# Kernel optimization log

Measured on AMD Instinct MI355X. Metric: run time of the kernel, lower is better.

The kernel has to match this reference:

```python
import jax, jax.numpy as jnp
import numpy as np
import math

# dims (scaled-down DeepSeek-MLA-style config)
DIM = 2048
NH = 16
QLR = 768       # dla_q_lora_rank
KVLR = 512      # dla_kv_lora_rank
DN = 128        # qk_nope_head_dim
DR = 64         # qk_rope_head_dim
DV = 128        # v_head_dim
QKH = DN + DR   # 192
BSZ = 1
SEQ = 2048
LAYER_IDX = 3
LAMBDA_INIT = 0.8 - 0.6 * math.exp(-0.3 * LAYER_IDX)
SCALE = QKH ** -0.5  # max_seq_len == original_seq_len -> no mscale correction
MAX_SCORE = 100.0


def apply_rope(x, cos, sin):
    # x: [b, s, h, d]; consecutive pairs (x[2i], x[2i+1]) form complex numbers
    xr, xi = x[..., 0::2], x[..., 1::2]
    c = cos[None, :, None, :]
    sn = sin[None, :, None, :]
    yr = xr * c - xi * sn
    yi = xr * sn + xi * c
    return jnp.stack([yr, yi], axis=-1).reshape(x.shape)


def setup_inputs() -> dict:
    key = jax.random.key(0)
    ks = jax.random.split(key, 12)
    x = jax.random.normal(ks[0], (BSZ, SEQ, DIM), dtype=jnp.float32)
    s = 0.02
    wq_a = jax.random.normal(ks[1], (QLR, DIM), dtype=jnp.float32) * s
    wq_b = jax.random.normal(ks[2], (NH * QKH, QLR), dtype=jnp.float32) * s
    wkv_a = jax.random.normal(ks[3], (KVLR + DR, DIM), dtype=jnp.float32) * s
    wkv_b = jax.random.normal(ks[4], (NH * (DN + DV), KVLR), dtype=jnp.float32) * s
    wo = jax.random.normal(ks[5], (DIM, NH * DV), dtype=jnp.float32) * s
    lambda_q_nope = jax.random.normal(ks[6], (DN,), dtype=jnp.float32) * 0.1
    lambda_q_rope = jax.random.normal(ks[7], (DR,), dtype=jnp.float32) * 0.1
    lambda_k_nope = jax.random.normal(ks[8], (DN,), dtype=jnp.float32) * 0.1
    lambda_k_rope = jax.random.normal(ks[9], (DR,), dtype=jnp.float32) * 0.1
    # rope frequencies
    inv_freq = 1.0 / (10000.0 ** (np.arange(0, DR, 2, dtype=np.float32) / DR))
    angles = np.arange(SEQ, dtype=np.float32)[:, None] * inv_freq[None, :]
    freqs_cos = jnp.asarray(np.cos(angles))
    freqs_sin = jnp.asarray(np.sin(angles))
    # causal mask (prefill, start_pos = 0)
    mask = jnp.where(jnp.tril(jnp.ones((SEQ, SEQ), dtype=bool)), 0.0, -1e9).astype(jnp.float32)
    return {
        'x': x, 'wq_a': wq_a, 'wq_b': wq_b, 'wkv_a': wkv_a, 'wkv_b': wkv_b, 'wo': wo,
        'lambda_q_nope': lambda_q_nope, 'lambda_q_rope': lambda_q_rope,
        'lambda_k_nope': lambda_k_nope, 'lambda_k_rope': lambda_k_rope,
        'freqs_cos': freqs_cos, 'freqs_sin': freqs_sin, 'mask': mask, 'start_pos': 0,
    }


def reference(x, wq_a, wq_b, wkv_a, wkv_b, wo,
              lambda_q_nope, lambda_q_rope, lambda_k_nope, lambda_k_rope,
              freqs_cos, freqs_sin, mask, start_pos):
    b, s, _ = x.shape
    # differential-attention lambda scalar
    lam = (jnp.exp(jnp.dot(lambda_q_nope, lambda_k_nope))
           - jnp.exp(jnp.dot(lambda_q_rope, lambda_k_rope)) + LAMBDA_INIT)
    # low-rank q projection
    q = (x @ wq_a.T) @ wq_b.T                    # [b, s, NH*QKH]
    q = q.reshape(b, s, NH, QKH)
    q_nope, q_pe = q[..., :DN], q[..., DN:]
    q_pe = apply_rope(q_pe, freqs_cos, freqs_sin)
    # compressed kv + shared rope key
    kv_full = x @ wkv_a.T                        # [b, s, KVLR + DR]
    kv, k_pe = kv_full[..., :KVLR], kv_full[..., KVLR:]
    k_pe = apply_rope(k_pe[:, :, None, :], freqs_cos, freqs_sin)  # [b, s, 1, DR]
    kvb = (kv @ wkv_b.T).reshape(b, s, NH, DN + DV)
    k_nope, v = kvb[..., :DN], kvb[..., DN:]
    q_full = jnp.concatenate([q_nope, q_pe], axis=-1)             # [b, s, NH, 192]
    k_full = jnp.concatenate([k_nope, jnp.broadcast_to(k_pe, (b, s, NH, DR))], axis=-1)
    # differential split into two halves of qk_head_dim//2 = 96
    H = QKH // 2
    q1, q2 = q_full[..., :H], q_full[..., H:]
    k1, k2 = k_full[..., :H], k_full[..., H:]
    s1 = jnp.einsum('bshd,bthd->bhst', q1, k1) * SCALE
    s2 = jnp.einsum('bshd,bthd->bhst', q2, k2) * SCALE
    s1 = jnp.clip(s1, -MAX_SCORE, MAX_SCORE) + mask[None, None]
    s2 = jnp.clip(s2, -MAX_SCORE, MAX_SCORE) + mask[None, None]
    attn = jax.nn.softmax(s1, axis=-1) - lam * jax.nn.softmax(s2, axis=-1)
    out = jnp.einsum('bhst,bthd->bshd', attn, v)  # [b, s, NH, DV]
    out = out * (1.0 - LAMBDA_INIT)
    return out.reshape(b, s, NH * DV) @ wo.T
```

## Files before the change

### kernel.cpp

```cpp
#include <hip/hip_runtime.h>
#include <stdint.h>

#define SEQ   2048
#define NH    16
#define DIMM  2048
#define QLR   768
#define KVLR  512
#define DN    128
#define DR    64
#define DV    128
#define QKH   192
#define KVPAD 640
#define SCALE_F 0.07216878364870323f
#define LAM_INIT 0.5560582f
#define C1F      0.4439418f
#define PSTR  36
#define DTHR  8.0f

typedef __attribute__((ext_vector_type(8))) uint16_t u16x8;
typedef __attribute__((ext_vector_type(8))) __bf16   bf16x8;
typedef __attribute__((ext_vector_type(4))) float    f32x4;

#define MFMA16(a,b,c) __builtin_amdgcn_mfma_f32_16x16x32_bf16((a),(b),(c),0,0,0)

__device__ __forceinline__ uint16_t f2bf(float f){ uint32_t x; __builtin_memcpy(&x,&f,4); return (uint16_t)((x + 0x7FFFu + ((x>>16)&1u))>>16); }
__device__ __forceinline__ float bfu(uint16_t u){ return (float)__builtin_bit_cast(__bf16, u); }
__device__ __forceinline__ bf16x8 ldfrag(const uint16_t* p){ return __builtin_bit_cast(bf16x8, *(const u16x8*)p); }
__device__ __forceinline__ void gload_lds16(const uint16_t* g, uint16_t* l){
  __builtin_amdgcn_global_load_lds((const __attribute__((address_space(1))) void*)g,
                                   (__attribute__((address_space(3))) void*)l, 16, 0, 0);
}
__device__ __forceinline__ void stor(uint16_t* p, float v){ *p = f2bf(v); }
__device__ __forceinline__ void stor(float* p, float v){ *p = v; }

__global__ void cvt(const float* __restrict__ in, uint16_t* __restrict__ outp){
  int i = (blockIdx.x*256 + threadIdx.x)*8;
  float4 a = *(const float4*)(in + i);
  float4 b = *(const float4*)(in + i + 4);
  u16x8 r;
  r[0]=f2bf(a.x); r[1]=f2bf(a.y); r[2]=f2bf(a.z); r[3]=f2bf(a.w);
  r[4]=f2bf(b.x); r[5]=f2bf(b.y); r[6]=f2bf(b.z); r[7]=f2bf(b.w);
  *(u16x8*)(outp + i) = r;
}

__global__ void pad_wkva(const float* __restrict__ in, uint16_t* __restrict__ outp){
  int idx = blockIdx.x*256 + threadIdx.x;
  int n = idx >> 11;
  outp[idx] = (n < 576) ? f2bf(in[idx]) : (uint16_t)0;
}

template <typename OT>
__global__ __launch_bounds__(256) void gemm_bt(const uint16_t* __restrict__ A, int lda,
                                               const uint16_t* __restrict__ B,
                                               OT* __restrict__ C, int ldc, int K)
{
  __shared__ __align__(16) uint16_t As[128*32];
  __shared__ __align__(16) uint16_t Bs[128*32];
  const int tid  = threadIdx.x;
  const int wid  = tid >> 6;
  const int lane = tid & 63;
  const int wr   = (wid >> 1) * 64;
  const int wc   = (wid & 1) * 64;
  const int srow = lane >> 2;
  const int scol = (lane & 3) * 8;
  const uint16_t* Abase = A + (size_t)(blockIdx.x * 128) * lda;
  const uint16_t* Bbase = B + (size_t)(blockIdx.y * 128) * K;
  f32x4 acc[4][4] = {};
  for (int k0 = 0; k0 < K; k0 += 32) {
    __syncthreads();
#pragma unroll
    for (int c = 0; c < 2; ++c) {
      int r = (wid*2 + c)*16 + srow;
      gload_lds16(Abase + (size_t)r*lda + k0 + scol, &As[(wid*2 + c)*512]);
      gload_lds16(Bbase + (size_t)r*K   + k0 + scol, &Bs[(wid*2 + c)*512]);
    }
    __syncthreads();
    bf16x8 af[4], bfr[4];
#pragma unroll
    for (int m = 0; m < 4; ++m)
      af[m] = ldfrag(&As[(wr + m*16 + (lane&15))*32 + ((lane>>4)*8)]);
#pragma unroll
    for (int n = 0; n < 4; ++n)
      bfr[n] = ldfrag(&Bs[(wc + n*16 + (lane&15))*32 + ((lane>>4)*8)]);
#pragma unroll
    for (int m = 0; m < 4; ++m)
#pragma unroll
      for (int n = 0; n < 4; ++n)
        acc[m][n] = MFMA16(af[m], bfr[n], acc[m][n]);
  }
  const int rbase = blockIdx.x*128 + wr + ((lane>>4)<<2);
  const int cbase = blockIdx.y*128 + wc + (lane&15);
#pragma unroll
  for (int m = 0; m < 4; ++m)
#pragma unroll
    for (int n = 0; n < 4; ++n)
#pragma unroll
      for (int r = 0; r < 4; ++r)
        stor(&C[(size_t)(rbase + m*16 + r)*ldc + cbase + n*16], acc[m][n][r]);
}

__global__ __launch_bounds__(256) void gemm_kvb(const uint16_t* __restrict__ A, int lda,
                                                const uint16_t* __restrict__ B,
                                                uint16_t* __restrict__ kfull,
                                                uint16_t* __restrict__ vtb, int K)
{
  __shared__ __align__(16) uint16_t As[128*32];
  __shared__ __align__(16) uint16_t Bs[128*32];
  const int tid  = threadIdx.x;
  const int wid  = tid >> 6;
  const int lane = tid & 63;
  const int wr   = (wid >> 1) * 64;
  const int wc   = (wid & 1) * 64;
  const int srow = lane >> 2;
  const int scol = (lane & 3) * 8;
  const uint16_t* Abase = A + (size_t)(blockIdx.x * 128) * lda;
  const uint16_t* Bbase = B + (size_t)(blockIdx.y * 128) * K;
  f32x4 acc[4][4] = {};
  for (int k0 = 0; k0 < K; k0 += 32) {
    __syncthreads();
#pragma unroll
    for (int c = 0; c < 2; ++c) {
      int r = (wid*2 + c)*16 + srow;
      gload_lds16(Abase + (size_t)r*lda + k0 + scol, &As[(wid*2 + c)*512]);
      gload_lds16(Bbase + (size_t)r*K   + k0 + scol, &Bs[(wid*2 + c)*512]);
    }
    __syncthreads();
    bf16x8 af[4], bfr[4];
#pragma unroll
    for (int m = 0; m < 4; ++m)
      af[m] = ldfrag(&As[(wr + m*16 + (lane&15))*32 + ((lane>>4)*8)]);
#pragma unroll
    for (int n = 0; n < 4; ++n)
      bfr[n] = ldfrag(&Bs[(wc + n*16 + (lane&15))*32 + ((lane>>4)*8)]);
#pragma unroll
    for (int m = 0; m < 4; ++m)
#pragma unroll
      for (int n = 0; n < 4; ++n)
        acc[m][n] = MFMA16(af[m], bfr[n], acc[m][n]);
  }
  const int rbase = blockIdx.x*128 + wr + ((lane>>4)<<2);
  const int cbase = blockIdx.y*128 + wc + (lane&15);
#pragma unroll
  for (int m = 0; m < 4; ++m)
#pragma unroll
    for (int n = 0; n < 4; ++n) {
      const int gcol = cbase + n*16;
      const int hh = gcol >> 8, d = gcol & 255;
#pragma unroll
      for (int r = 0; r < 4; ++r) {
        const int t = rbase + m*16 + r;
        if (d < DN) kfull[((size_t)hh*SEQ + t)*QKH + d] = f2bf(acc[m][n][r]);
        else        vtb[((size_t)hh*DV + (d - DN))*SEQ + t] = f2bf(acc[m][n][r]);
      }
    }
}

__global__ void lam_kernel(const float* lqn, const float* lqr,
                           const float* lkn, const float* lkr, float* outp){
  if (threadIdx.x == 0 && blockIdx.x == 0) {
    float d1 = 0.f, d2 = 0.f;
    for (int i = 0; i < DN; ++i) d1 += lqn[i] * lkn[i];
    for (int i = 0; i < DR; ++i) d2 += lqr[i] * lkr[i];
    outp[0] = __expf(d1) - __expf(d2) + LAM_INIT;
  }
}

__global__ void rope_q(uint16_t* __restrict__ q, const float* __restrict__ cs,
                       const float* __restrict__ sn){
  int idx = blockIdx.x*256 + threadIdx.x;
  int j = idx & 31, hh = (idx>>5) & 15, s = idx >> 9;
  uint16_t* p = q + (size_t)s*(NH*QKH) + hh*QKH + DN + 2*j;
  float xr = bfu(p[0]), xi = bfu(p[1]);
  float c = cs[s*32+j], si = sn[s*32+j];
  p[0] = f2bf(xr*c - xi*si);
  p[1] = f2bf(xr*si + xi*c);
}

__global__ void rope_k(const uint16_t* __restrict__ kvf, const float* __restrict__ cs,
                       const float* __restrict__ sn, uint16_t* __restrict__ kfull){
  int idx = blockIdx.x*256 + threadIdx.x;
  int j = idx & 31, t = (idx>>5) & 2047, hh = idx >> 16;
  float xr = bfu(kvf[(size_t)t*KVPAD + KVLR + 2*j]);
  float xi = bfu(kvf[(size_t)t*KVPAD + KVLR + 2*j + 1]);
  float c = cs[t*32+j], si = sn[t*32+j];
  uint16_t* p = kfull + ((size_t)hh*SEQ + t)*QKH + DN + 2*j;
  p[0] = f2bf(xr*c - xi*si);
  p[1] = f2bf(xr*si + xi*c);
}

__global__ __launch_bounds__(256) __attribute__((amdgpu_waves_per_eu(2)))
void attn_kernel(
    const uint16_t* __restrict__ q,
    const uint16_t* __restrict__ kf,
    const uint16_t* __restrict__ vt,
    const float* __restrict__ lamp,
    uint16_t* __restrict__ o)
{
  __shared__ __align__(16) uint16_t P_lds[4][4][16*PSTR];
  __shared__ float R_lds[2][64*41];
  const int b  = blockIdx.x;
  const int h  = b & 15;
  const int c  = b >> 4;
  const int wid  = threadIdx.x >> 6;
  const int lane = threadIdx.x & 63;
  const int l15 = lane & 15;
  const int lhi = lane >> 4;
  const int subrow = lhi * 4;
  const int qrow0 = c * 16;
  const int kend  = qrow0 + 16;
  const float lam = lamp[0];

  bf16x8 qf[6];
  {
    const uint16_t* qbase = q + (size_t)(qrow0 + l15)*(NH*QKH) + h*QKH + lhi*8;
#pragma unroll
    for (int kb = 0; kb < 6; ++kb) qf[kb] = ldfrag(qbase + kb*32);
  }
  f32x4 O1[8] = {}, O2[8] = {};
  float m1[4], m2[4], l1[4], l2[4];
#pragma unroll
  for (int r = 0; r < 4; ++r) { m1[r] = m2[r] = -1e30f; l1[r] = l2[r] = 0.f; }

  const uint16_t* kbase = kf + (size_t)h*SEQ*QKH;
  const uint16_t* vbase = vt + (size_t)h*DV*SEQ;

  auto loadK = [&](bf16x8 (&k0)[6], bf16x8 (&k1)[6], int t0){
    const uint16_t* kp0 = kbase + (size_t)(t0 + l15)*QKH + lhi*8;
    const uint16_t* kp1 = kp0 + (size_t)16*QKH;
#pragma unroll
    for (int kb = 0; kb < 6; ++kb) { k0[kb] = ldfrag(kp0 + kb*32); k1[kb] = ldfrag(kp1 + kb*32); }
  };
  auto loadV = [&](bf16x8 (&vf)[8], int t0){
#pragma unroll
    for (int n = 0; n < 8; ++n) vf[n] = ldfrag(vbase + (size_t)(n*16 + l15)*SEQ + t0 + lhi*8);
  };
  auto qk = [&](bf16x8 (&k0)[6], bf16x8 (&k1)[6], f32x4 (&s1)[2], f32x4 (&s2)[2]){
    __builtin_amdgcn_s_setprio(1);
#pragma unroll
    for (int kb = 0; kb < 3; ++kb) { s1[0] = MFMA16(qf[kb], k0[kb], s1[0]); s1[1] = MFMA16(qf[kb], k1[kb], s1[1]); }
#pragma unroll
    for (int kb = 3; kb < 6; ++kb) { s2[0] = MFMA16(qf[kb], k0[kb], s2[0]); s2[1] = MFMA16(qf[kb], k1[kb], s2[1]); }
    __builtin_amdgcn_s_setprio(0);
  };
  auto smax = [&](f32x4 (&s1)[2], f32x4 (&s2)[2], int t0, bool MASKED,
                  uint16_t* pa, uint16_t* pb){
#pragma unroll
    for (int half = 0; half < 2; ++half)
#pragma unroll
      for (int r = 0; r < 4; ++r) {
        float v1 = fminf(fmaxf(s1[half][r]*SCALE_F, -100.f), 100.f);
        float v2 = fminf(fmaxf(s2[half][r]*SCALE_F, -100.f), 100.f);
        if (MASKED && (t0 + half*16 + l15 > qrow0 + subrow + r)) { v1 = -1e30f; v2 = -1e30f; }
        s1[half][r] = v1; s2[half][r] = v2;
      }
    float t1[4], t2[4];
#pragma unroll
    for (int r = 0; r < 4; ++r) { t1[r] = fmaxf(s1[0][r], s1[1][r]); t2[r] = fmaxf(s2[0][r], s2[1][r]); }
#pragma unroll
    for (int off = 1; off < 16; off <<= 1)
#pragma unroll
      for (int r = 0; r < 4; ++r) {
        t1[r] = fmaxf(t1[r], __shfl_xor(t1[r], off, 64));
        t2[r] = fmaxf(t2[r], __shfl_xor(t2[r], off, 64));
      }
    bool ok1 = (t1[0] <= m1[0]+DTHR) && (t1[1] <= m1[1]+DTHR) && (t1[2] <= m1[2]+DTHR) && (t1[3] <= m1[3]+DTHR);
    if (!__all(ok1)) {
#pragma unroll
      for (int r = 0; r < 4; ++r) {
        float mn = fmaxf(m1[r], t1[r]);
        float cr = __expf(m1[r] - mn);
        m1[r] = mn; l1[r] *= cr;
#pragma unroll
        for (int n = 0; n < 8; ++n) O1[n][r] *= cr;
      }
    }
    bool ok2 = (t2[0] <= m2[0]+DTHR) && (t2[1] <= m2[1]+DTHR) && (t2[2] <= m2[2]+DTHR) && (t2[3] <= m2[3]+DTHR);
    if (!__all(ok2)) {
#pragma unroll
      for (int r = 0; r < 4; ++r) {
        float mn = fmaxf(m2[r], t2[r]);
        float cr = __expf(m2[r] - mn);
        m2[r] = mn; l2[r] *= cr;
#pragma unroll
        for (int n = 0; n < 8; ++n) O2[n][r] *= cr;
      }
    }
    float rs1[4], rs2[4];
#pragma unroll
    for (int r = 0; r < 4; ++r) {
      float p10 = __expf(s1[0][r] - m1[r]), p11 = __expf(s1[1][r] - m1[r]);
      float p20 = __expf(s2[0][r] - m2[r]), p21 = __expf(s2[1][r] - m2[r]);
      pa[(subrow + r)*PSTR +      l15] = f2bf(p10);
      pa[(subrow + r)*PSTR + 16 + l15] = f2bf(p11);
      pb[(subrow + r)*PSTR +      l15] = f2bf(p20);
      pb[(subrow + r)*PSTR + 16 + l15] = f2bf(p21);
      rs1[r] = p10 + p11; rs2[r] = p20 + p21;
    }
#pragma unroll
    for (int off = 1; off < 16; off <<= 1)
#pragma unroll
      for (int r = 0; r < 4; ++r) {
        rs1[r] += __shfl_xor(rs1[r], off, 64);
        rs2[r] += __shfl_xor(rs2[r], off, 64);
      }
#pragma unroll
    for (int r = 0; r < 4; ++r) { l1[r] += rs1[r]; l2[r] += rs2[r]; }
  };
  auto pv = [&](bf16x8 (&vf)[8], const uint16_t* pa, const uint16_t* pb){
    bf16x8 pf0 = ldfrag(&pa[l15*PSTR + lhi*8]);
    bf16x8 pf1 = ldfrag(&pb[l15*PSTR + lhi*8]);
    __builtin_amdgcn_s_setprio(1);
#pragma unroll
    for (int n = 0; n < 8; ++n) {
      O1[n] = MFMA16(pf0, vf[n], O1[n]);
      O2[n] = MFMA16(pf1, vf[n], O2[n]);
    }
    __builtin_amdgcn_s_setprio(0);
  };

  uint16_t* plA0 = &P_lds[wid][0][0]; uint16_t* plA1 = &P_lds[wid][1][0];
  uint16_t* plB0 = &P_lds[wid][2][0]; uint16_t* plB1 = &P_lds[wid][3][0];

  const int n_tiles = (kend + 31) >> 5;
  const int nm = n_tiles - 1;

  bf16x8 kr0[6], kr1[6], vfa[8], vfb[8];
  int i = wid;
  for (; i + 4 < nm; i += 8) {
    const int ta = i*32, tb = (i+4)*32;
    loadK(kr0, kr1, ta);
    loadV(vfa, ta);
    f32x4 sA1[2] = {}, sA2[2] = {};
    qk(kr0, kr1, sA1, sA2);
    loadK(kr0, kr1, tb);
    smax(sA1, sA2, ta, false, plA0, plA1);
    f32x4 sB1[2] = {}, sB2[2] = {};
    qk(kr0, kr1, sB1, sB2);
    loadV(vfb, tb);
    smax(sB1, sB2, tb, false, plB0, plB1);
    asm volatile("s_waitcnt lgkmcnt(0)" ::: "memory");
    __builtin_amdgcn_sched_barrier(0);
    pv(vfa, plA0, plA1);
    pv(vfb, plB0, plB1);
  }
  if (i < nm) {
    loadK(kr0, kr1, i*32);
    loadV(vfa, i*32);
    f32x4 s1[2] = {}, s2[2] = {};
    qk(kr0, kr1, s1, s2);
    smax(s1, s2, i*32, false, plA0, plA1);
    asm volatile("s_waitcnt lgkmcnt(0)" ::: "memory");
    __builtin_amdgcn_sched_barrier(0);
    pv(vfa, plA0, plA1);
  }
  if ((nm & 3) == wid) {
    loadK(kr0, kr1, nm*32);
    loadV(vfa, nm*32);
    f32x4 s1[2] = {}, s2[2] = {};
    qk(kr0, kr1, s1, s2);
    smax(s1, s2, nm*32, true, plA0, plA1);
    asm volatile("s_waitcnt lgkmcnt(0)" ::: "memory");
    __builtin_amdgcn_sched_barrier(0);
    pv(vfa, plA0, plA1);
  }

  auto write_state = [&](float* buf, const float* mm, const float* ll, const f32x4* O){
    float* p = buf + lane*41;
#pragma unroll
    for (int r = 0; r < 4; ++r) { p[r] = mm[r]; p[4+r] = ll[r]; }
#pragma unroll
    for (int n = 0; n < 8; ++n)
#pragma unroll
      for (int r = 0; r < 4; ++r) p[8 + n*4 + r] = O[n][r];
  };
  auto merge_state = [&](const float* buf, float* mm, float* ll, f32x4* O){
    const float* p = buf + lane*41;
    float ca[4], cb[4];
#pragma unroll
    for (int r = 0; r < 4; ++r) {
      float mo = p[r], lo = p[4+r];
      float mn = fmaxf(mm[r], mo);
      ca[r] = __expf(mm[r] - mn); cb[r] = __expf(mo - mn);
      mm[r] = mn; ll[r] = ll[r]*ca[r] + lo*cb[r];
    }
#pragma unroll
    for (int n = 0; n < 8; ++n)
#pragma unroll
      for (int r = 0; r < 4; ++r) O[n][r] = O[n][r]*ca[r] + p[8 + n*4 + r]*cb[r];
  };

  if (wid >= 2) write_state(R_lds[wid-2], m1, l1, O1);
  __syncthreads();
  if (wid < 2)  merge_state(R_lds[wid], m1, l1, O1);
  __syncthreads();
  if (wid >= 2) write_state(R_lds[wid-2], m2, l2, O2);
  __syncthreads();
  if (wid < 2)  merge_state(R_lds[wid], m2, l2, O2);
  __syncthreads();
  if (wid == 1) { write_state(R_lds[0], m1, l1, O1); write_state(R_lds[1], m2, l2, O2); }
  __syncthreads();
  if (wid == 0) {
    merge_state(R_lds[0], m1, l1, O1);
    merge_state(R_lds[1], m2, l2, O2);
#pragma unroll
    for (int r = 0; r < 4; ++r) {
      float inv1 = 1.f / l1[r], inv2 = lam / l2[r];
#pragma unroll
      for (int n = 0; n < 8; ++n) {
        float val = (O1[n][r]*inv1 - O2[n][r]*inv2) * C1F;
        o[(size_t)(qrow0 + subrow + r)*(NH*DV) + h*DV + n*16 + l15] = f2bf(val);
      }
    }
  }
}

extern "C" void kernel_launch(void* const* d_in, const int* in_sizes, int n_in,
                              void* d_out, int out_size, void* d_ws, size_t ws_size,
                              hipStream_t stream)
{
  const float* x     = (const float*)d_in[0];
  const float* wq_a  = (const float*)d_in[1];
  const float* wq_b  = (const float*)d_in[2];
  const float* wkv_a = (const float*)d_in[3];
  const float* wkv_b = (const float*)d_in[4];
  const float* wo    = (const float*)d_in[5];
  const float* lqn   = (const float*)d_in[6];
  const float* lqr   = (const float*)d_in[7];
  const float* lkn   = (const float*)d_in[8];
  const float* lkr   = (const float*)d_in[9];
  const float* fcos  = (const float*)d_in[10];
  const float* fsin  = (const float*)d_in[11];

  char* ws = (char*)d_ws;
  size_t off = 0;
  float*    lam    = (float*)(ws + off);  off += 256;
  uint16_t* xb     = (uint16_t*)(ws + off); off += (size_t)DIMM*DIMM*2;
  uint16_t* wqab   = (uint16_t*)(ws + off); off += (size_t)QLR*DIMM*2;
  uint16_t* wqbb   = (uint16_t*)(ws + off); off += (size_t)NH*QKH*QLR*2;
  uint16_t* wkvap  = (uint16_t*)(ws + off); off += (size_t)KVPAD*DIMM*2;
  uint16_t* wkvbb  = (uint16_t*)(ws + off); off += (size_t)4096*KVLR*2;
  uint16_t* wob    = (uint16_t*)(ws + off); off += (size_t)DIMM*DIMM*2;
  uint16_t* qlat   = (uint16_t*)(ws + off); off += (size_t)SEQ*QLR*2;
  uint16_t* qbuf   = (uint16_t*)(ws + off); off += (size_t)SEQ*NH*QKH*2;
  uint16_t* kvfull = (uint16_t*)(ws + off); off += (size_t)SEQ*KVPAD*2;
  uint16_t* kfull  = (uint16_t*)(ws + off); off += (size_t)NH*SEQ*QKH*2;
  uint16_t* vtb    = (uint16_t*)(ws + off); off += (size_t)NH*DV*SEQ*2;
  uint16_t* attn   = (uint16_t*)(ws + off); off += (size_t)SEQ*NH*DV*2;

  lam_kernel<<<1, 64, 0, stream>>>(lqn, lqr, lkn, lkr, lam);
  cvt<<<2048, 256, 0, stream>>>(x, xb);
  cvt<<< 768, 256, 0, stream>>>(wq_a, wqab);
  cvt<<<1152, 256, 0, stream>>>(wq_b, wqbb);
  cvt<<<1024, 256, 0, stream>>>(wkv_b, wkvbb);
  cvt<<<2048, 256, 0, stream>>>(wo, wob);
  pad_wkva<<<5120, 256, 0, stream>>>(wkv_a, wkvap);

  gemm_bt<<<dim3(16, 6), 256, 0, stream>>>(xb, DIMM, wqab, qlat, QLR, DIMM);
  gemm_bt<<<dim3(16, 24), 256, 0, stream>>>(qlat, QLR, wqbb, qbuf, NH*QKH, QLR);
  rope_q<<<4096, 256, 0, stream>>>(qbuf, fcos, fsin);
  gemm_bt<<<dim3(16, 5), 256, 0, stream>>>(xb, DIMM, wkvap, kvfull, KVPAD, DIMM);
  gemm_kvb<<<dim3(16, 32), 256, 0, stream>>>(kvfull, KVPAD, wkvbb, kfull, vtb, KVLR);
  rope_k<<<4096, 256, 0, stream>>>(kvfull, fcos, fsin, kfull);
  attn_kernel<<<2048, 256, 0, stream>>>(qbuf, kfull, vtb, lam, attn);
  gemm_bt<<<dim3(16, 16), 256, 0, stream>>>(attn, NH*DV, wob, (float*)d_out, DIMM, DIMM);
}
```

Baseline: 399.9 us.

## Share LDS-staged K/V tiles across four query-row waves in attention

The attention kernel now gives each block 64 query rows (16 per wave) instead of 16 rows with the KV range split across waves. K and V tiles are staged once per block into double-buffered shared memory and reused by all four waves, which drops the cross-wave softmax-state merge and divides global K/V traffic by four. Block order is paired (j and 47-j) to balance the causal workload, and the grid shrinks from 2048 to 512 blocks. The cost is a block-wide barrier every tile, idle waves on diagonal tiles, and fewer blocks to fill the CUs.

New measurement: 403.8 us. No clear change (+1.0%).

```diff
diff --git a/kernel.cpp b/kernel.cpp
--- a/kernel.cpp
+++ b/kernel.cpp
@@ -16,6 +16,8 @@
 #define C1F      0.4439418f
 #define PSTR  36
 #define DTHR  8.0f
+#define KPAD  200
+#define VPAD  40
 
 typedef __attribute__((ext_vector_type(8))) uint16_t u16x8;
 typedef __attribute__((ext_vector_type(8))) __bf16   bf16x8;
@@ -188,7 +190,7 @@
   p[1] = f2bf(xr*si + xi*c);
 }
 
-__global__ __launch_bounds__(256) __attribute__((amdgpu_waves_per_eu(2)))
+__global__ __launch_bounds__(256)
 void attn_kernel(
     const uint16_t* __restrict__ q,
     const uint16_t* __restrict__ kf,
@@ -196,19 +198,28 @@
     const float* __restrict__ lamp,
     uint16_t* __restrict__ o)
 {
-  __shared__ __align__(16) uint16_t P_lds[4][4][16*PSTR];
-  __shared__ float R_lds[2][64*41];
+  __shared__ __align__(16) uint16_t Kl[2][32*KPAD];
+  __shared__ __align__(16) uint16_t Vl[2][128*VPAD];
+  __shared__ __align__(16) uint16_t P_lds[4][2][16*PSTR];
   const int b  = blockIdx.x;
   const int h  = b & 15;
-  const int c  = b >> 4;
-  const int wid  = threadIdx.x >> 6;
-  const int lane = threadIdx.x & 63;
+  const int j  = b >> 4;
+  const int qb = (j < 16) ? j : 47 - j;
+  const int tid  = threadIdx.x;
+  const int wid  = tid >> 6;
+  const int lane = tid & 63;
   const int l15 = lane & 15;
   const int lhi = lane >> 4;
   const int subrow = lhi * 4;
-  const int qrow0 = c * 16;
-  const int kend  = qrow0 + 16;
+  const int qrow0 = qb*64 + wid*16;
+  const int ntiles = 2*qb + 2;
   const float lam = lamp[0];
+
+  const int krow = tid >> 3, kc = tid & 7;
+  const int vrow = tid >> 1, vc = tid & 1;
+
+  const uint16_t* kbase = kf + (size_t)h*SEQ*QKH;
+  const uint16_t* vbase = vt + (size_t)h*DV*SEQ;
 
   bf16x8 qf[6];
   {
@@ -221,195 +232,140 @@
 #pragma unroll
   for (int r = 0; r < 4; ++r) { m1[r] = m2[r] = -1e30f; l1[r] = l2[r] = 0.f; }
 
-  const uint16_t* kbase = kf + (size_t)h*SEQ*QKH;
-  const uint16_t* vbase = vt + (size_t)h*DV*SEQ;
-
-  auto loadK = [&](bf16x8 (&k0)[6], bf16x8 (&k1)[6], int t0){
-    const uint16_t* kp0 = kbase + (size_t)(t0 + l15)*QKH + lhi*8;
-    const uint16_t* kp1 = kp0 + (size_t)16*QKH;
-#pragma unroll
-    for (int kb = 0; kb < 6; ++kb) { k0[kb] = ldfrag(kp0 + kb*32); k1[kb] = ldfrag(kp1 + kb*32); }
+  uint16_t* pl0 = &P_lds[wid][0][0];
+  uint16_t* pl1 = &P_lds[wid][1][0];
+
+  u16x8 kr[3], vr[2];
+  auto stage_load = [&](int t0){
+    const uint16_t* kp = kbase + (size_t)(t0 + krow)*QKH;
+#pragma unroll
+    for (int i = 0; i < 3; ++i) kr[i] = *(const u16x8*)(kp + (kc + 8*i)*8);
+    const uint16_t* vp = vbase + (size_t)vrow*SEQ + t0;
+#pragma unroll
+    for (int i = 0; i < 2; ++i) vr[i] = *(const u16x8*)(vp + (vc + 2*i)*8);
   };
-  auto loadV = [&](bf16x8 (&vf)[8], int t0){
-#pragma unroll
-    for (int n = 0; n < 8; ++n) vf[n] = ldfrag(vbase + (size_t)(n*16 + l15)*SEQ + t0 + lhi*8);
+  auto stage_write = [&](int buf){
+    uint16_t* kd = &Kl[buf][krow*KPAD];
+#pragma unroll
+    for (int i = 0; i < 3; ++i) *(u16x8*)(kd + (kc + 8*i)*8) = kr[i];
+    uint16_t* vd = &Vl[buf][vrow*VPAD];
+#pragma unroll
+    for (int i = 0; i < 2; ++i) *(u16x8*)(vd + (vc + 2*i)*8) = vr[i];
   };
-  auto qk = [&](bf16x8 (&k0)[6], bf16x8 (&k1)[6], f32x4 (&s1)[2], f32x4 (&s2)[2]){
-    __builtin_amdgcn_s_setprio(1);
-#pragma unroll
-    for (int kb = 0; kb < 3; ++kb) { s1[0] = MFMA16(qf[kb], k0[kb], s1[0]); s1[1] = MFMA16(qf[kb], k1[kb], s1[1]); }
-#pragma unroll
-    for (int kb = 3; kb < 6; ++kb) { s2[0] = MFMA16(qf[kb], k0[kb], s2[0]); s2[1] = MFMA16(qf[kb], k1[kb], s2[1]); }
-    __builtin_amdgcn_s_setprio(0);
-  };
-  auto smax = [&](f32x4 (&s1)[2], f32x4 (&s2)[2], int t0, bool MASKED,
-                  uint16_t* pa, uint16_t* pb){
-#pragma unroll
-    for (int half = 0; half < 2; ++half)
+
+  stage_load(0);
+  stage_write(0);
+  __syncthreads();
+
+  int cur = 0;
+  for (int ti = 0; ti < ntiles; ++ti) {
+    const int t0 = ti * 32;
+    const bool pre = (ti + 1 < ntiles);
+    if (pre) stage_load(t0 + 32);
+
+    if (t0 <= qrow0 + 15) {
+      const bool MASKED = (t0 + 32 > qrow0);
+      f32x4 s1[2] = {}, s2[2] = {};
+      __builtin_amdgcn_s_setprio(1);
+#pragma unroll
+      for (int half = 0; half < 2; ++half) {
+        const uint16_t* kl = &Kl[cur][(half*16 + l15)*KPAD + lhi*8];
+#pragma unroll
+        for (int kb = 0; kb < 3; ++kb) s1[half] = MFMA16(qf[kb], ldfrag(kl + kb*32), s1[half]);
+#pragma unroll
+        for (int kb = 3; kb < 6; ++kb) s2[half] = MFMA16(qf[kb], ldfrag(kl + kb*32), s2[half]);
+      }
+      __builtin_amdgcn_s_setprio(0);
+
+#pragma unroll
+      for (int half = 0; half < 2; ++half)
+#pragma unroll
+        for (int r = 0; r < 4; ++r) {
+          float v1 = fminf(fmaxf(s1[half][r]*SCALE_F, -100.f), 100.f);
+          float v2 = fminf(fmaxf(s2[half][r]*SCALE_F, -100.f), 100.f);
+          if (MASKED && (t0 + half*16 + l15 > qrow0 + subrow + r)) { v1 = -1e30f; v2 = -1e30f; }
+          s1[half][r] = v1; s2[half][r] = v2;
+        }
+      float t1[4], t2[4];
+#pragma unroll
+      for (int r = 0; r < 4; ++r) { t1[r] = fmaxf(s1[0][r], s1[1][r]); t2[r] = fmaxf(s2[0][r], s2[1][r]); }
+#pragma unroll
+      for (int off = 1; off < 16; off <<= 1)
+#pragma unroll
+        for (int r = 0; r < 4; ++r) {
+          t1[r] = fmaxf(t1[r], __shfl_xor(t1[r], off, 64));
+          t2[r] = fmaxf(t2[r], __shfl_xor(t2[r], off, 64));
+        }
+      bool ok1 = (t1[0] <= m1[0]+DTHR) && (t1[1] <= m1[1]+DTHR) && (t1[2] <= m1[2]+DTHR) && (t1[3] <= m1[3]+DTHR);
+      if (!__all(ok1)) {
+#pragma unroll
+        for (int r = 0; r < 4; ++r) {
+          float mn = fmaxf(m1[r], t1[r]);
+          float cr = __expf(m1[r] - mn);
+          m1[r] = mn; l1[r] *= cr;
+#pragma unroll
+          for (int n = 0; n < 8; ++n) O1[n][r] *= cr;
+        }
+      }
+      bool ok2 = (t2[0] <= m2[0]+DTHR) && (t2[1] <= m2[1]+DTHR) && (t2[2] <= m2[2]+DTHR) && (t2[3] <= m2[3]+DTHR);
+      if (!__all(ok2)) {
+#pragma unroll
+        for (int r = 0; r < 4; ++r) {
+          float mn = fmaxf(m2[r], t2[r]);
+          float cr = __expf(m2[r] - mn);
+          m2[r] = mn; l2[r] *= cr;
+#pragma unroll
+          for (int n = 0; n < 8; ++n) O2[n][r] *= cr;
+        }
+      }
+      float rs1[4], rs2[4];
 #pragma unroll
       for (int r = 0; r < 4; ++r) {
-        float v1 = fminf(fmaxf(s1[half][r]*SCALE_F, -100.f), 100.f);
-        float v2 = fminf(fmaxf(s2[half][r]*SCALE_F, -100.f), 100.f);
-        if (MASKED && (t0 + half*16 + l15 > qrow0 + subrow + r)) { v1 = -1e30f; v2 = -1e30f; }
-        s1[half][r] = v1; s2[half][r] = v2;
-      }
-    float t1[4], t2[4];
-#pragma unroll
-    for (int r = 0; r < 4; ++r) { t1[r] = fmaxf(s1[0][r], s1[1][r]); t2[r] = fmaxf(s2[0][r], s2[1][r]); }
-#pragma unroll
-    for (int off = 1; off < 16; off <<= 1)
-#pragma unroll
-      for (int r = 0; r < 4; ++r) {
-        t1[r] = fmaxf(t1[r], __shfl_xor(t1[r], off, 64));
-        t2[r] = fmaxf(t2[r], __shfl_xor(t2[r], off, 64));
-      }
-    bool ok1 = (t1[0] <= m1[0]+DTHR) && (t1[1] <= m1[1]+DTHR) && (t1[2] <= m1[2]+DTHR) && (t1[3] <= m1[3]+DTHR);
-    if (!__all(ok1)) {
-#pragma unroll
-      for (int r = 0; r < 4; ++r) {
-        float mn = fmaxf(m1[r], t1[r]);
-        float cr = __expf(m1[r] - mn);
-        m1[r] = mn; l1[r] *= cr;
-#pragma unroll
-        for (int n = 0; n < 8; ++n) O1[n][r] *= cr;
-      }
+        float p10 = __expf(s1[0][r] - m1[r]), p11 = __expf(s1[1][r] - m1[r]);
+        float p20 = __expf(s2[0][r] - m2[r]), p21 = __expf(s2[1][r] - m2[r]);
+        pl0[(subrow + r)*PSTR +      l15] = f2bf(p10);
+        pl0[(subrow + r)*PSTR + 16 + l15] = f2bf(p11);
+        pl1[(subrow + r)*PSTR +      l15] = f2bf(p20);
+        pl1[(subrow + r)*PSTR + 16 + l15] = f2bf(p21);
+        rs1[r] = p10 + p11; rs2[r] = p20 + p21;
+      }
+#pragma unroll
+      for (int off = 1; off < 16; off <<= 1)
+#pragma unroll
+        for (int r = 0; r < 4; ++r) {
+          rs1[r] += __shfl_xor(rs1[r], off, 64);
+          rs2[r] += __shfl_xor(rs2[r], off, 64);
+        }
+#pragma unroll
+      for (int r = 0; r < 4; ++r) { l1[r] += rs1[r]; l2[r] += rs2[r]; }
+
+      asm volatile("s_waitcnt lgkmcnt(0)" ::: "memory");
+      __builtin_amdgcn_sched_barrier(0);
+
+      bf16x8 pf0 = ldfrag(&pl0[l15*PSTR + lhi*8]);
+      bf16x8 pf1 = ldfrag(&pl1[l15*PSTR + lhi*8]);
+      __builtin_amdgcn_s_setprio(1);
+#pragma unroll
+      for (int n = 0; n < 8; ++n) {
+        bf16x8 vf = ldfrag(&Vl[cur][(n*16 + l15)*VPAD + lhi*8]);
+        O1[n] = MFMA16(pf0, vf, O1[n]);
+        O2[n] = MFMA16(pf1, vf, O2[n]);
+      }
+      __builtin_amdgcn_s_setprio(0);
     }
-    bool ok2 = (t2[0] <= m2[0]+DTHR) && (t2[1] <= m2[1]+DTHR) && (t2[2] <= m2[2]+DTHR) && (t2[3] <= m2[3]+DTHR);
-    if (!__all(ok2)) {
-#pragma unroll
-      for (int r = 0; r < 4; ++r) {
-        float mn = fmaxf(m2[r], t2[r]);
-        float cr = __expf(m2[r] - mn);
-        m2[r] = mn; l2[r] *= cr;
-#pragma unroll
-        for (int n = 0; n < 8; ++n) O2[n][r] *= cr;
-      }
-    }
-    float rs1[4], rs2[4];
-#pragma unroll
-    for (int r = 0; r < 4; ++r) {
-      float p10 = __expf(s1[0][r] - m1[r]), p11 = __expf(s1[1][r] - m1[r]);
-      float p20 = __expf(s2[0][r] - m2[r]), p21 = __expf(s2[1][r] - m2[r]);
-      pa[(subrow + r)*PSTR +      l15] = f2bf(p10);
-      pa[(subrow + r)*PSTR + 16 + l15] = f2bf(p11);
-      pb[(subrow + r)*PSTR +      l15] = f2bf(p20);
-      pb[(subrow + r)*PSTR + 16 + l15] = f2bf(p21);
-      rs1[r] = p10 + p11; rs2[r] = p20 + p21;
-    }
-#pragma unroll
-    for (int off = 1; off < 16; off <<= 1)
-#pragma unroll
-      for (int r = 0; r < 4; ++r) {
-        rs1[r] += __shfl_xor(rs1[r], off, 64);
-        rs2[r] += __shfl_xor(rs2[r], off, 64);
-      }
-#pragma unroll
-    for (int r = 0; r < 4; ++r) { l1[r] += rs1[r]; l2[r] += rs2[r]; }
-  };
-  auto pv = [&](bf16x8 (&vf)[8], const uint16_t* pa, const uint16_t* pb){
-    bf16x8 pf0 = ldfrag(&pa[l15*PSTR + lhi*8]);
-    bf16x8 pf1 = ldfrag(&pb[l15*PSTR + lhi*8]);
-    __builtin_amdgcn_s_setprio(1);
+
+    if (pre) stage_write(cur ^ 1);
+    __syncthreads();
+    cur ^= 1;
+  }
+
+#pragma unroll
+  for (int r = 0; r < 4; ++r) {
+    float inv1 = 1.f / l1[r], inv2 = lam / l2[r];
 #pragma unroll
     for (int n = 0; n < 8; ++n) {
-      O1[n] = MFMA16(pf0, vf[n], O1[n]);
-      O2[n] = MFMA16(pf1, vf[n], O2[n]);
-    }
-    __builtin_amdgcn_s_setprio(0);
-  };
-
-  uint16_t* plA0 = &P_lds[wid][0][0]; uint16_t* plA1 = &P_lds[wid][1][0];
-  uint16_t* plB0 = &P_lds[wid][2][0]; uint16_t* plB1 = &P_lds[wid][3][0];
-
-  const int n_tiles = (kend + 31) >> 5;
-  const int nm = n_tiles - 1;
-
-  bf16x8 kr0[6], kr1[6], vfa[8], vfb[8];
-  int i = wid;
-  for (; i + 4 < nm; i += 8) {
-    const int ta = i*32, tb = (i+4)*32;
-    loadK(kr0, kr1, ta);
-    loadV(vfa, ta);
-    f32x4 sA1[2] = {}, sA2[2] = {};
-    qk(kr0, kr1, sA1, sA2);
-    loadK(kr0, kr1, tb);
-    smax(sA1, sA2, ta, false, plA0, plA1);
-    f32x4 sB1[2] = {}, sB2[2] = {};
-    qk(kr0, kr1, sB1, sB2);
-    loadV(vfb, tb);
-    smax(sB1, sB2, tb, false, plB0, plB1);
-    asm volatile("s_waitcnt lgkmcnt(0)" ::: "memory");
-    __builtin_amdgcn_sched_barrier(0);
-    pv(vfa, plA0, plA1);
-    pv(vfb, plB0, plB1);
-  }
-  if (i < nm) {
-    loadK(kr0, kr1, i*32);
-    loadV(vfa, i*32);
-    f32x4 s1[2] = {}, s2[2] = {};
-    qk(kr0, kr1, s1, s2);
-    smax(s1, s2, i*32, false, plA0, plA1);
-    asm volatile("s_waitcnt lgkmcnt(0)" ::: "memory");
-    __builtin_amdgcn_sched_barrier(0);
-    pv(vfa, plA0, plA1);
-  }
-  if ((nm & 3) == wid) {
-    loadK(kr0, kr1, nm*32);
-    loadV(vfa, nm*32);
-    f32x4 s1[2] = {}, s2[2] = {};
-    qk(kr0, kr1, s1, s2);
-    smax(s1, s2, nm*32, true, plA0, plA1);
-    asm volatile("s_waitcnt lgkmcnt(0)" ::: "memory");
-    __builtin_amdgcn_sched_barrier(0);
-    pv(vfa, plA0, plA1);
-  }
-
-  auto write_state = [&](float* buf, const float* mm, const float* ll, const f32x4* O){
-    float* p = buf + lane*41;
-#pragma unroll
-    for (int r = 0; r < 4; ++r) { p[r] = mm[r]; p[4+r] = ll[r]; }
-#pragma unroll
-    for (int n = 0; n < 8; ++n)
-#pragma unroll
-      for (int r = 0; r < 4; ++r) p[8 + n*4 + r] = O[n][r];
-  };
-  auto merge_state = [&](const float* buf, float* mm, float* ll, f32x4* O){
-    const float* p = buf + lane*41;
-    float ca[4], cb[4];
-#pragma unroll
-    for (int r = 0; r < 4; ++r) {
-      float mo = p[r], lo = p[4+r];
-      float mn = fmaxf(mm[r], mo);
-      ca[r] = __expf(mm[r] - mn); cb[r] = __expf(mo - mn);
-      mm[r] = mn; ll[r] = ll[r]*ca[r] + lo*cb[r];
-    }
-#pragma unroll
-    for (int n = 0; n < 8; ++n)
-#pragma unroll
-      for (int r = 0; r < 4; ++r) O[n][r] = O[n][r]*ca[r] + p[8 + n*4 + r]*cb[r];
-  };
-
-  if (wid >= 2) write_state(R_lds[wid-2], m1, l1, O1);
-  __syncthreads();
-  if (wid < 2)  merge_state(R_lds[wid], m1, l1, O1);
-  __syncthreads();
-  if (wid >= 2) write_state(R_lds[wid-2], m2, l2, O2);
-  __syncthreads();
-  if (wid < 2)  merge_state(R_lds[wid], m2, l2, O2);
-  __syncthreads();
-  if (wid == 1) { write_state(R_lds[0], m1, l1, O1); write_state(R_lds[1], m2, l2, O2); }
-  __syncthreads();
-  if (wid == 0) {
-    merge_state(R_lds[0], m1, l1, O1);
-    merge_state(R_lds[1], m2, l2, O2);
-#pragma unroll
-    for (int r = 0; r < 4; ++r) {
-      float inv1 = 1.f / l1[r], inv2 = lam / l2[r];
-#pragma unroll
-      for (int n = 0; n < 8; ++n) {
-        float val = (O1[n][r]*inv1 - O2[n][r]*inv2) * C1F;
-        o[(size_t)(qrow0 + subrow + r)*(NH*DV) + h*DV + n*16 + l15] = f2bf(val);
-      }
+      float val = (O1[n][r]*inv1 - O2[n][r]*inv2) * C1F;
+      o[(size_t)(qrow0 + subrow + r)*(NH*DV) + h*DV + n*16 + l15] = f2bf(val);
     }
   }
 }
@@ -461,6 +417,6 @@
   gemm_bt<<<dim3(16, 5), 256, 0, stream>>>(xb, DIMM, wkvap, kvfull, KVPAD, DIMM);
   gemm_kvb<<<dim3(16, 32), 256, 0, stream>>>(kvfull, KVPAD, wkvbb, kfull, vtb, KVLR);
   rope_k<<<4096, 256, 0, stream>>>(kvfull, fcos, fsin, kfull);
-  attn_kernel<<<2048, 256, 0, stream>>>(qbuf, kfull, vtb, lam, attn);
+  attn_kernel<<<512, 256, 0, stream>>>(qbuf, kfull, vtb, lam, attn);
   gemm_bt<<<dim3(16, 16), 256, 0, stream>>>(attn, NH*DV, wob, (float*)d_out, DIMM, DIMM);
 }
```
